# Performance work log

Measured on AMD Instinct MI355X. Metric: run time of the kernel, lower is better.

Reference implementation:

```python
import jax, jax.numpy as jnp
import numpy as np

H = 10          # hidden_dim
OUT = 100       # linear output (charset logits)
STEPS = 30      # decoder steps
START = 1.0     # Alphabet.start_integer
NL = 3          # num_layers
B, L, TD, AD = 8192, 32, 63, 1
IN = TD + AD


def setup_inputs() -> dict:
    key = jax.random.key(0)
    ks = iter(jax.random.split(key, 64))
    s = 0.3
    d = {}
    d["families"] = jnp.zeros((B,), jnp.int32)
    d["languages"] = jnp.zeros((B,), jnp.int32)
    d["tags"] = jax.random.uniform(next(ks), (B, TD), jnp.float32)
    d["lemmata"] = jax.random.uniform(next(ks), (B, L), jnp.float32)
    for pre in ("enc", "dec"):
        for l in range(NL):
            din = IN if l == 0 else H
            d[f"{pre}_W_ih{l}"] = jax.random.normal(next(ks), (4 * H, din), jnp.float32) * s
            d[f"{pre}_W_hh{l}"] = jax.random.normal(next(ks), (4 * H, H), jnp.float32) * s
            d[f"{pre}_b_ih{l}"] = jax.random.normal(next(ks), (4 * H,), jnp.float32) * s
            d[f"{pre}_b_hh{l}"] = jax.random.normal(next(ks), (4 * H,), jnp.float32) * s
    d["lin_W"] = jax.random.normal(next(ks), (OUT, H), jnp.float32) * s
    d["lin_b"] = jnp.zeros((OUT,), jnp.float32)
    return d


def _lstm_cell(layers, h, c, x):
    # torch LSTM gate order: i, f, g, o. Dropout inactive in eval mode.
    nh, nc, inp = [], [], x
    for (W_ih, W_hh, b_ih, b_hh), hl, cl in zip(layers, h, c):
        g = inp @ W_ih.T + hl @ W_hh.T + b_ih + b_hh  # (B, 4H)
        i_, f_, g_, o_ = jnp.split(g, 4, axis=-1)
        cl = jax.nn.sigmoid(f_) * cl + jax.nn.sigmoid(i_) * jnp.tanh(g_)
        hl = jax.nn.sigmoid(o_) * jnp.tanh(cl)
        nh.append(hl); nc.append(cl); inp = hl
    return tuple(nh), tuple(nc), inp


def _forward(tags, lemmata, enc, dec, lin_W, lin_b):
    Bb, Ll = lemmata.shape
    # time-major encoder input: feature order [char, tags...] -> (L, B, 1+TD)
    xs = jnp.concatenate([lemmata.T[:, :, None],
                          jnp.broadcast_to(tags[None], (Ll, Bb, tags.shape[1]))], axis=-1)
    h = tuple(jnp.zeros((Bb, H), lemmata.dtype) for _ in range(NL))
    c = h

    def estep(carry, x):
        hh, cc = carry
        hh, cc, _ = _lstm_cell(enc, hh, cc, x)
        return (hh, cc), None

    (h, c), _ = jax.lax.scan(estep, (h, c), xs)

    tok = jnp.full((Bb,), START, lemmata.dtype)

    def dstep(carry, _):
        hh, cc, t = carry
        x = jnp.concatenate([t[:, None], tags], axis=-1)  # (B, 1+TD)
        hh, cc, y = _lstm_cell(dec, hh, cc, x)
        probs = jax.nn.sigmoid(y @ lin_W.T + lin_b)       # (B, 100)
        nt = jax.lax.stop_gradient(jnp.argmax(probs, axis=-1))
        return (hh, cc, nt.astype(t.dtype)), (probs, nt)

    _, (probs, toks) = jax.lax.scan(dstep, (h, c, tok), None, length=STEPS)
    return jnp.transpose(probs, (1, 0, 2)), toks.T  # (B,30,100), (B,30)


def reference(families, languages, tags, lemmata,
              enc_W_ih0, enc_W_hh0, enc_b_ih0, enc_b_hh0,
              enc_W_ih1, enc_W_hh1, enc_b_ih1, enc_b_hh1,
              enc_W_ih2, enc_W_hh2, enc_b_ih2, enc_b_hh2,
              dec_W_ih0, dec_W_hh0, dec_b_ih0, dec_b_hh0,
              dec_W_ih1, dec_W_hh1, dec_b_ih1, dec_b_hh1,
              dec_W_ih2, dec_W_hh2, dec_b_ih2, dec_b_hh2,
              lin_W, lin_b):
    enc = ((enc_W_ih0, enc_W_hh0, enc_b_ih0, enc_b_hh0),
           (enc_W_ih1, enc_W_hh1, enc_b_ih1, enc_b_hh1),
           (enc_W_ih2, enc_W_hh2, enc_b_ih2, enc_b_hh2))
    dec = ((dec_W_ih0, dec_W_hh0, dec_b_ih0, dec_b_hh0),
           (dec_W_ih1, dec_W_hh1, dec_b_ih1, dec_b_hh1),
           (dec_W_ih2, dec_W_hh2, dec_b_ih2, dec_b_hh2))
    return _forward(tags, lemmata, enc, dec, lin_W, lin_b)
```

## Files before the change

kernel.cpp:

```cpp
#include <hip/hip_runtime.h>
#include <cmath>
#include <stdint.h>

#define DEV __device__ __forceinline__

typedef float v2f __attribute__((ext_vector_type(2)));

static DEV float fast_exp2(float x) { return __builtin_amdgcn_exp2f(x); }
static DEV float fast_rcp(float x) { return __builtin_amdgcn_rcpf(x); }

#define LOG2E 1.4426950408889634f

static DEV float rdl(float x, int l) {
  return __int_as_float(__builtin_amdgcn_readlane(__float_as_int(x), l));
}
static DEV int rdli(float x, int l) {
  return __builtin_amdgcn_readlane(__float_as_int(x), l);
}
static DEV uint64_t pack2(int lo, int hi) {
  return ((uint64_t)(uint32_t)hi << 32) | (uint32_t)lo;
}

static DEV void pkfma(v2f& acc, v2f w, uint64_t h) {
  asm("v_pk_fma_f32 %0, %1, %2, %0" : "+v"(acc) : "v"(w), "s"(h));
}

template <int K>
static DEV float qb(float x) {
  return __int_as_float(
      __builtin_amdgcn_update_dpp(0, __float_as_int(x), K * 0x55, 0xF, 0xF, true));
}

template <int CTRL>
static DEV float dppmax(float x) {
  float o = __int_as_float(
      __builtin_amdgcn_update_dpp(0, __float_as_int(x), CTRL, 0xF, 0xF, true));
  return fmaxf(x, o);
}

static DEV float wavemax_bcast(float m) {
  m = dppmax<0x111>(m);
  m = dppmax<0x112>(m);
  m = dppmax<0x114>(m);
  m = dppmax<0x118>(m);
  m = dppmax<0x142>(m);
  m = dppmax<0x143>(m);
  return rdl(m, 63);
}

struct KP {
  const float* tags; const float* lem;
  const float* eWih0; const float* eWhh0; const float* ebih0; const float* ebhh0;
  const float* eWih1; const float* eWhh1; const float* ebih1; const float* ebhh1;
  const float* eWih2; const float* eWhh2; const float* ebih2; const float* ebhh2;
  const float* dWih0; const float* dWhh0; const float* dbih0; const float* dbhh0;
  const float* dWih1; const float* dWhh1; const float* dbih1; const float* dbhh1;
  const float* dWih2; const float* dWhh2; const float* dbih2; const float* dbhh2;
  const float* linW; const float* linb;
  float* outp; float* outt;
  int B;
};

__global__ __launch_bounds__(256) void seq2seq_kernel(KP P) {
  const int tid = threadIdx.x;
  const int lane = tid & 63;
  const int b = blockIdx.x * 4 + (tid >> 6);
  if (b >= P.B) return;

  const int jq = lane >> 2;
  const int kg = lane & 3;
  const int jj = (jq < 10) ? jq : 9;
  const int row = kg * 10 + jj;

  const float kc = (kg == 2) ? (-2.0f * LOG2E) : (-LOG2E);
  const float am = (kg == 2) ? 2.0f : 1.0f;
  const float ab = (kg == 2) ? -1.0f : 0.0f;

  auto act = [&](float g) -> float {
    float y = fast_rcp(1.0f + fast_exp2(g * kc));
    return fmaf(am, y, ab);
  };

  float tv = (lane < 63) ? P.tags[(size_t)b * 63 + lane] : 0.0f;
  float lemv = (lane < 32) ? P.lem[(size_t)b * 32 + lane] : 0.0f;

  float pre0 = P.ebih0[row] + P.ebhh0[row];
  float dpre0 = P.dbih0[row] + P.dbhh0[row];
  float ew0c, dw0c;
  {
    const float4* e4 = (const float4*)P.eWih0 + row * 16;
    const float4* d4 = (const float4*)P.dWih0 + row * 16;
    float4 we = e4[0], wd = d4[0];
    ew0c = we.x; dw0c = wd.x;
    float t0 = rdl(tv, 0), t1 = rdl(tv, 1), t2 = rdl(tv, 2);
    pre0 = fmaf(we.y, t0, pre0); pre0 = fmaf(we.z, t1, pre0); pre0 = fmaf(we.w, t2, pre0);
    dpre0 = fmaf(wd.y, t0, dpre0); dpre0 = fmaf(wd.z, t1, dpre0); dpre0 = fmaf(wd.w, t2, dpre0);
#pragma unroll
    for (int c = 1; c < 16; c++) {
      float4 e = e4[c], d = d4[c];
      int dd = 4 * c - 1;
      float u0 = rdl(tv, dd), u1 = rdl(tv, dd + 1), u2 = rdl(tv, dd + 2), u3 = rdl(tv, dd + 3);
      pre0 = fmaf(e.x, u0, pre0); pre0 = fmaf(e.y, u1, pre0);
      pre0 = fmaf(e.z, u2, pre0); pre0 = fmaf(e.w, u3, pre0);
      dpre0 = fmaf(d.x, u0, dpre0); dpre0 = fmaf(d.y, u1, dpre0);
      dpre0 = fmaf(d.z, u2, dpre0); dpre0 = fmaf(d.w, u3, dpre0);
    }
  }

  v2f ehh0[5], eih1[5], ehh1[5], eih2[5], ehh2[5];
  {
    const v2f* a0 = (const v2f*)(P.eWhh0 + row * 10);
    const v2f* a1 = (const v2f*)(P.eWih1 + row * 10);
    const v2f* a2 = (const v2f*)(P.eWhh1 + row * 10);
    const v2f* a3 = (const v2f*)(P.eWih2 + row * 10);
    const v2f* a4 = (const v2f*)(P.eWhh2 + row * 10);
#pragma unroll
    for (int q = 0; q < 5; q++) {
      ehh0[q] = a0[q]; eih1[q] = a1[q]; ehh1[q] = a2[q];
      eih2[q] = a3[q]; ehh2[q] = a4[q];
    }
  }
  float pre1 = P.ebih1[row] + P.ebhh1[row];
  float pre2 = P.ebih2[row] + P.ebhh2[row];

  uint64_t h0[5], h1[5], h2[5];
#pragma unroll
  for (int q = 0; q < 5; q++) { h0[q] = 0; h1[q] = 0; h2[q] = 0; }
  float c0 = 0.0f, c1 = 0.0f, c2 = 0.0f;

  auto upd = [&](float a, float& c, uint64_t (&h)[5]) {
    float a0 = qb<0>(a);
    float a1 = qb<1>(a);
    float a2 = qb<2>(a);
    float a3 = qb<3>(a);
    c = fmaf(a1, c, a0 * a2);
    float y = fast_rcp(1.0f + fast_exp2(c * (-2.0f * LOG2E)));
    float hv = a3 * fmaf(2.0f, y, -1.0f);
#pragma unroll
    for (int q = 0; q < 5; q++) h[q] = pack2(rdli(hv, 8 * q), rdli(hv, 8 * q + 4));
  };

  auto step = [&](float x, const v2f (&wh0)[5], const v2f (&wi1)[5],
                  const v2f (&wh1)[5], const v2f (&wi2)[5], const v2f (&wh2)[5],
                  float w0c, float p0_, float p1_, float p2_) {
    v2f a{fmaf(w0c, x, p0_), 0.0f};
#pragma unroll
    for (int q = 0; q < 5; q++) pkfma(a, wh0[q], h0[q]);
    upd(act(a.x + a.y), c0, h0);

    v2f aa{p1_, 0.0f}, bb{0.0f, 0.0f};
#pragma unroll
    for (int q = 0; q < 5; q++) { pkfma(aa, wi1[q], h0[q]); pkfma(bb, wh1[q], h1[q]); }
    upd(act((aa.x + aa.y) + (bb.x + bb.y)), c1, h1);

    v2f cc_{p2_, 0.0f}, dd{0.0f, 0.0f};
#pragma unroll
    for (int q = 0; q < 5; q++) { pkfma(cc_, wi2[q], h1[q]); pkfma(dd, wh2[q], h2[q]); }
    upd(act((cc_.x + cc_.y) + (dd.x + dd.y)), c2, h2);
  };

  for (int t = 0; t < 32; t++) {
    step(rdl(lemv, t), ehh0, eih1, ehh1, eih2, ehh2, ew0c, pre0, pre1, pre2);
  }

  {
    const v2f* a0 = (const v2f*)(P.dWhh0 + row * 10);
    const v2f* a1 = (const v2f*)(P.dWih1 + row * 10);
    const v2f* a2 = (const v2f*)(P.dWhh1 + row * 10);
    const v2f* a3 = (const v2f*)(P.dWih2 + row * 10);
    const v2f* a4 = (const v2f*)(P.dWhh2 + row * 10);
#pragma unroll
    for (int q = 0; q < 5; q++) {
      ehh0[q] = a0[q]; eih1[q] = a1[q]; ehh1[q] = a2[q];
      eih2[q] = a3[q]; ehh2[q] = a4[q];
    }
  }
  pre1 = P.dbih1[row] + P.dbhh1[row];
  pre2 = P.dbih2[row] + P.dbhh2[row];

  const int lr2 = (lane < 36) ? (64 + lane) : 99;
  v2f lw0[5], lw1[5];
  {
    const v2f* a0 = (const v2f*)(P.linW + lane * 10);
    const v2f* a1 = (const v2f*)(P.linW + lr2 * 10);
#pragma unroll
    for (int q = 0; q < 5; q++) { lw0[q] = a0[q]; lw1[q] = a1[q]; }
  }
  float lb0 = P.linb[lane];
  float lb1 = (lane < 36) ? P.linb[lr2] : -1e30f;

  float* op0 = P.outp + (size_t)b * 3000;
  float tok = 1.0f;
  float tokv = 0.0f;

  for (int s = 0; s < 30; s++) {
    step(tok, ehh0, eih1, ehh1, eih2, ehh2, dw0c, dpre0, pre1, pre2);

    v2f za{lb0, 0.0f}, zb{lb1, 0.0f};
#pragma unroll
    for (int q = 0; q < 5; q++) { pkfma(za, lw0[q], h2[q]); pkfma(zb, lw1[q], h2[q]); }
    float z0 = za.x + za.y, z1 = zb.x + zb.y;
    float p0 = fast_rcp(1.0f + fast_exp2(z0 * (-LOG2E)));
    float p1 = fast_rcp(1.0f + fast_exp2(z1 * (-LOG2E)));

    float* op = op0 + s * 100;
    op[lane] = p0;
    if (lane < 36) op[64 + lane] = p1;

    float vm = wavemax_bcast(fmaxf(p0, p1));
    unsigned long long m0 = __ballot(p0 == vm);
    unsigned long long m1 = __ballot(p1 == vm);
    int im = m0 ? (int)__builtin_ctzll(m0) : 64 + (int)__builtin_ctzll(m1);
    tok = (float)im;
    tokv = (lane == s) ? tok : tokv;
  }

  if (lane < 30) P.outt[(size_t)b * 30 + lane] = tokv;
}

extern "C" void kernel_launch(void* const* d_in, const int* in_sizes, int n_in,
                              void* d_out, int out_size, void* d_ws, size_t ws_size,
                              hipStream_t stream) {
  KP P;
  P.tags = (const float*)d_in[2];
  P.lem = (const float*)d_in[3];
  P.eWih0 = (const float*)d_in[4];  P.eWhh0 = (const float*)d_in[5];
  P.ebih0 = (const float*)d_in[6];  P.ebhh0 = (const float*)d_in[7];
  P.eWih1 = (const float*)d_in[8];  P.eWhh1 = (const float*)d_in[9];
  P.ebih1 = (const float*)d_in[10]; P.ebhh1 = (const float*)d_in[11];
  P.eWih2 = (const float*)d_in[12]; P.eWhh2 = (const float*)d_in[13];
  P.ebih2 = (const float*)d_in[14]; P.ebhh2 = (const float*)d_in[15];
  P.dWih0 = (const float*)d_in[16]; P.dWhh0 = (const float*)d_in[17];
  P.dbih0 = (const float*)d_in[18]; P.dbhh0 = (const float*)d_in[19];
  P.dWih1 = (const float*)d_in[20]; P.dWhh1 = (const float*)d_in[21];
  P.dbih1 = (const float*)d_in[22]; P.dbhh1 = (const float*)d_in[23];
  P.dWih2 = (const float*)d_in[24]; P.dWhh2 = (const float*)d_in[25];
  P.dbih2 = (const float*)d_in[26]; P.dbhh2 = (const float*)d_in[27];
  P.linW = (const float*)d_in[28];
  P.linb = (const float*)d_in[29];

  const int B = in_sizes[3] / 32;
  P.B = B;
  P.outp = (float*)d_out;
  P.outt = P.outp + (size_t)B * 3000;

  const int blocks = (B + 3) / 4;
  seq2seq_kernel<<<dim3(blocks), dim3(256), 0, stream>>>(P);
}
```

Baseline: 155.6 us.

## Broadcast hidden state via ds_bpermute and stage linear weights in LDS

```diff
diff --git a/kernel.cpp b/kernel.cpp
--- a/kernel.cpp
+++ b/kernel.cpp
@@ -14,15 +14,13 @@
 static DEV float rdl(float x, int l) {
   return __int_as_float(__builtin_amdgcn_readlane(__float_as_int(x), l));
 }
-static DEV int rdli(float x, int l) {
-  return __builtin_amdgcn_readlane(__float_as_int(x), l);
-}
-static DEV uint64_t pack2(int lo, int hi) {
-  return ((uint64_t)(uint32_t)hi << 32) | (uint32_t)lo;
-}
-
-static DEV void pkfma(v2f& acc, v2f w, uint64_t h) {
-  asm("v_pk_fma_f32 %0, %1, %2, %0" : "+v"(acc) : "v"(w), "s"(h));
+
+static DEV void pkfma(v2f& acc, v2f w, v2f h) {
+  asm("v_pk_fma_f32 %0, %1, %2, %0" : "+v"(acc) : "v"(w), "v"(h));
+}
+
+static DEV float bcast(int byteidx, float v) {
+  return __int_as_float(__builtin_amdgcn_ds_bpermute(byteidx, __float_as_int(v)));
 }
 
 template <int K>
@@ -61,10 +59,14 @@
   int B;
 };
 
-__global__ __launch_bounds__(256) void seq2seq_kernel(KP P) {
+__global__ __launch_bounds__(256, 4) void seq2seq_kernel(KP P) {
   const int tid = threadIdx.x;
   const int lane = tid & 63;
   const int b = blockIdx.x * 4 + (tid >> 6);
+
+  __shared__ float slin[1000];
+  for (int i = tid; i < 1000; i += 256) slin[i] = P.linW[i];
+  __syncthreads();
   if (b >= P.B) return;
 
   const int jq = lane >> 2;
@@ -123,12 +125,12 @@
   float pre1 = P.ebih1[row] + P.ebhh1[row];
   float pre2 = P.ebih2[row] + P.ebhh2[row];
 
-  uint64_t h0[5], h1[5], h2[5];
-#pragma unroll
-  for (int q = 0; q < 5; q++) { h0[q] = 0; h1[q] = 0; h2[q] = 0; }
+  v2f h0[5], h1[5], h2[5];
+#pragma unroll
+  for (int q = 0; q < 5; q++) { h0[q] = v2f{0, 0}; h1[q] = v2f{0, 0}; h2[q] = v2f{0, 0}; }
   float c0 = 0.0f, c1 = 0.0f, c2 = 0.0f;
 
-  auto upd = [&](float a, float& c, uint64_t (&h)[5]) {
+  auto upd = [&](float a, float& c, v2f (&h)[5]) {
     float a0 = qb<0>(a);
     float a1 = qb<1>(a);
     float a2 = qb<2>(a);
@@ -137,7 +139,10 @@
     float y = fast_rcp(1.0f + fast_exp2(c * (-2.0f * LOG2E)));
     float hv = a3 * fmaf(2.0f, y, -1.0f);
 #pragma unroll
-    for (int q = 0; q < 5; q++) h[q] = pack2(rdli(hv, 8 * q), rdli(hv, 8 * q + 4));
+    for (int q = 0; q < 5; q++) {
+      h[q].x = bcast(32 * q, hv);
+      h[q].y = bcast(32 * q + 16, hv);
+    }
   };
 
   auto step = [&](float x, const v2f (&wh0)[5], const v2f (&wi1)[5],
@@ -179,13 +184,8 @@
   pre2 = P.dbih2[row] + P.dbhh2[row];
 
   const int lr2 = (lane < 36) ? (64 + lane) : 99;
-  v2f lw0[5], lw1[5];
-  {
-    const v2f* a0 = (const v2f*)(P.linW + lane * 10);
-    const v2f* a1 = (const v2f*)(P.linW + lr2 * 10);
-#pragma unroll
-    for (int q = 0; q < 5; q++) { lw0[q] = a0[q]; lw1[q] = a1[q]; }
-  }
+  const v2f* lp0 = (const v2f*)(slin + lane * 10);
+  const v2f* lp1 = (const v2f*)(slin + lr2 * 10);
   float lb0 = P.linb[lane];
   float lb1 = (lane < 36) ? P.linb[lr2] : -1e30f;
 
@@ -198,7 +198,7 @@
 
     v2f za{lb0, 0.0f}, zb{lb1, 0.0f};
 #pragma unroll
-    for (int q = 0; q < 5; q++) { pkfma(za, lw0[q], h2[q]); pkfma(zb, lw1[q], h2[q]); }
+    for (int q = 0; q < 5; q++) { pkfma(za, lp0[q], h2[q]); pkfma(zb, lp1[q], h2[q]); }
     float z0 = za.x + za.y, z1 = zb.x + zb.y;
     float p0 = fast_rcp(1.0f + fast_exp2(z0 * (-LOG2E)));
     float p1 = fast_rcp(1.0f + fast_exp2(z1 * (-LOG2E)));
```

After: 206.5 us. 1.33x slower.
